# Kernel tuning notes

Measured on AMD Instinct MI355X. Metric: run time of the kernel, lower is better.

## Reference

```python
import jax, jax.numpy as jnp
import numpy as np

EPS = 1e-5
HID = 32
FUSED = 33 * 33 * 33  # 35937


def _subnet(x, gamma, beta, W1, b1, W2, b2, W3, b3):
    # BatchNorm1d in training mode: batch mean / biased variance
    mu = jnp.mean(x, axis=0)
    var = jnp.mean((x - mu) ** 2, axis=0)
    xn = (x - mu) / jnp.sqrt(var + EPS) * gamma + beta
    h = jax.nn.relu(xn @ W1 + b1)
    h = jax.nn.relu(h @ W2 + b2)
    return jax.nn.relu(h @ W3 + b3)


def _subnet_params(key, in_dim):
    ks = jax.random.split(key, 6)
    s_in = 1.0 / np.sqrt(in_dim)
    s_h = 1.0 / np.sqrt(HID)
    return dict(
        gamma=jnp.ones((in_dim,), jnp.float32),
        beta=jnp.zeros((in_dim,), jnp.float32),
        W1=jax.random.uniform(ks[0], (in_dim, HID), jnp.float32, -s_in, s_in),
        b1=jax.random.uniform(ks[1], (HID,), jnp.float32, -s_in, s_in),
        W2=jax.random.uniform(ks[2], (HID, HID), jnp.float32, -s_h, s_h),
        b2=jax.random.uniform(ks[3], (HID,), jnp.float32, -s_h, s_h),
        W3=jax.random.uniform(ks[4], (HID, HID), jnp.float32, -s_h, s_h),
        b3=jax.random.uniform(ks[5], (HID,), jnp.float32, -s_h, s_h),
    )


def setup_inputs() -> dict:
    key = jax.random.key(0)
    ks = jax.random.split(key, 10)
    B = 8192
    inp = {
        'US_x': jax.random.normal(ks[0], (B, 1024), jnp.float32),
        'CDFI_x': jax.random.normal(ks[1], (B, 1024), jnp.float32),
        'marker_x': jax.random.normal(ks[2], (B, 10), jnp.float32),
    }
    for pref, k, d in (('us', ks[3], 1024), ('cd', ks[4], 1024), ('mk', ks[5], 10)):
        for n, v in _subnet_params(k, d).items():
            inp[f'{pref}_{n}'] = v
    s1 = 1.0 / np.sqrt(FUSED)
    s2 = 1.0 / np.sqrt(33)
    inp['Wf1'] = jax.random.uniform(ks[6], (FUSED, 33), jnp.float32, -s1, s1)
    inp['bf1'] = jax.random.uniform(ks[7], (33,), jnp.float32, -s1, s1)
    inp['Wf2'] = jax.random.uniform(ks[8], (33, 5), jnp.float32, -s2, s2)
    inp['bf2'] = jax.random.uniform(ks[9], (5,), jnp.float32, -s2, s2)
    return inp


def reference(US_x, CDFI_x, marker_x,
              us_gamma, us_beta, us_W1, us_b1, us_W2, us_b2, us_W3, us_b3,
              cd_gamma, cd_beta, cd_W1, cd_b1, cd_W2, cd_b2, cd_W3, cd_b3,
              mk_gamma, mk_beta, mk_W1, mk_b1, mk_W2, mk_b2, mk_W3, mk_b3,
              Wf1, bf1, Wf2, bf2):
    B = US_x.shape[0]
    us_h = _subnet(US_x, us_gamma, us_beta, us_W1, us_b1, us_W2, us_b2, us_W3, us_b3)
    cd_h = _subnet(CDFI_x, cd_gamma, cd_beta, cd_W1, cd_b1, cd_W2, cd_b2, cd_W3, cd_b3)
    mk_h = _subnet(marker_x, mk_gamma, mk_beta, mk_W1, mk_b1, mk_W2, mk_b2, mk_W3, mk_b3)
    ones = jnp.ones((B, 1), jnp.float32)
    us1 = jnp.concatenate([ones, us_h], axis=1)   # [B,33]
    cd1 = jnp.concatenate([ones, cd_h], axis=1)   # [B,33]
    mk1 = jnp.concatenate([ones, mk_h], axis=1)   # [B,33]
    # fused[b,k,j,i] = mk1[b,k] * cd1[b,j] * us1[b,i]; flattened row-major
    fused = jnp.einsum('bk,bj,bi->bkji', mk1, cd1, us1).reshape(B, FUSED)
    h = jax.nn.relu(fused @ Wf1 + bf1)
    return jax.nn.sigmoid(h @ Wf2 + bf2)
```

## Files before the change

kernel.cpp:

```cpp
#include <hip/hip_runtime.h>
#include <hip/hip_bf16.h>
#include <math.h>

typedef __hip_bfloat16 bf16;
typedef __attribute__((ext_vector_type(4))) float f32x4;
typedef __attribute__((ext_vector_type(8))) short s16x8;

#define NB 8192
#define KP 1152
#define NP 1152
#define NK 36


struct SubP {
    const float* x; const float* gamma; const float* beta;
    const float* W1; const float* b1; const float* W2; const float* b2;
    const float* W3; const float* b3;
    float* sum; float* sumsq; float* a; float* b1p; float* hout;
    int F;
};
struct SubP3 { SubP s[3]; };

__global__ void __launch_bounds__(256) stats3_kernel(SubP3 P) {
    const SubP p = P.s[blockIdx.z];
    int t = threadIdx.x;
    int row0 = blockIdx.x * 64;
    if (p.F == 1024) {
        f32x4 s = {0.f, 0.f, 0.f, 0.f}, s2 = {0.f, 0.f, 0.f, 0.f};
        const float* xp = p.x + (size_t)row0 * 1024 + t * 4;
        #pragma unroll 8
        for (int r = 0; r < 64; r++) {
            f32x4 v = *(const f32x4*)(xp + (size_t)r * 1024);
            s += v; s2 += v * v;
        }
        int f = t * 4;
        #pragma unroll
        for (int e = 0; e < 4; e++) {
            atomicAdd(&p.sum[f + e], s[e]);
            atomicAdd(&p.sumsq[f + e], s2[e]);
        }
    } else {
        __shared__ float ls[16], ls2[16];
        if (t < 16) { ls[t] = 0.f; ls2[t] = 0.f; }
        __syncthreads();
        int F = p.F;
        for (int idx = t; idx < 64 * F; idx += 256) {
            float v = p.x[(size_t)row0 * F + idx];
            int f = idx % 10;
            atomicAdd(&ls[f], v);
            atomicAdd(&ls2[f], v * v);
        }
        __syncthreads();
        if (t < F) { atomicAdd(&p.sum[t], ls[t]); atomicAdd(&p.sumsq[t], ls2[t]); }
    }
}

__global__ void prep3_kernel(SubP3 P) {
    const SubP p = P.s[blockIdx.y];
    int f0 = blockIdx.x * 32;
    if (f0 >= p.F) return;
    int t = threadIdx.x;
    __shared__ float c_sh[32];
    __shared__ float red[8][33];
    int fc = p.F - f0; if (fc > 32) fc = 32;
    if (t < 32) {
        float c = 0.f;
        if (t < fc) {
            int f = f0 + t;
            float mu  = p.sum[f]   * (1.f / 8192.f);
            float var = p.sumsq[f] * (1.f / 8192.f) - mu * mu;
            float a = p.gamma[f] * rsqrtf(var + 1e-5f);
            p.a[f] = a;
            c = p.beta[f] - mu * a;
        }
        c_sh[t] = c;
    }
    __syncthreads();
    int h = t & 31, g = t >> 5;
    float s = 0.f;
    for (int fi = g; fi < fc; fi += 8)
        s += c_sh[fi] * p.W1[(size_t)(f0 + fi) * 32 + h];
    red[g][h] = s;
    __syncthreads();
    if (t < 32) {
        float tot = 0.f;
        #pragma unroll
        for (int gg = 0; gg < 8; gg++) tot += red[gg][t];
        atomicAdd(&p.b1p[t], tot);
    }
}

__global__ void __launch_bounds__(256) subnet3_kernel(SubP3 P) {
    const SubP p = P.s[blockIdx.y];
    const int F = p.F;
    __shared__ float smem[8832];
    float* Red = smem;
    float* H1  = smem + 3456;
    float* W23 = smem + 4608;
    float* H2  = smem;

    int t = threadIdx.x;
    int row0 = blockIdx.x * 32;
    int kg = t >> 6;
    int lane = t & 63;
    int hg = lane & 7, h0 = hg * 4;
    int rg = (lane >> 3) & 3;
    int ks = lane >> 5;

    float acc[4][8] = {};

    if (F == 1024) {
        float* Xt = smem;
        float* Wt = smem + 4224;
        int xr = t >> 3, xc = (t & 7) * 16;
        int wk = t >> 1, wh = (t & 1) * 16;
        const float* xbase = p.x + (size_t)row0 * 1024;
        f32x4 xp[4], wp[4]; float av;
        #pragma unroll
        for (int i = 0; i < 4; i++) xp[i] = *(const f32x4*)&xbase[(size_t)xr * 1024 + xc + i * 4];
        #pragma unroll
        for (int i = 0; i < 4; i++) wp[i] = *(const f32x4*)&p.W1[(size_t)wk * 32 + wh + i * 4];
        av = p.a[wk];
        int kb = (kg * 2 + ks) * 16;
        for (int c = 0; c < 8; c++) {
            __syncthreads();
            #pragma unroll
            for (int i = 0; i < 4; i++) *(f32x4*)&Xt[xr * 132 + xc + i * 4] = xp[i];
            #pragma unroll
            for (int i = 0; i < 4; i++) *(f32x4*)&Wt[wk * 36 + wh + i * 4] = wp[i] * av;
            if (c < 7) {
                int k0 = (c + 1) * 128;
                #pragma unroll
                for (int i = 0; i < 4; i++) xp[i] = *(const f32x4*)&xbase[(size_t)xr * 1024 + k0 + xc + i * 4];
                #pragma unroll
                for (int i = 0; i < 4; i++) wp[i] = *(const f32x4*)&p.W1[(size_t)(k0 + wk) * 32 + wh + i * 4];
                av = p.a[k0 + wk];
            }
            __syncthreads();
            #pragma unroll
            for (int s = 0; s < 4; s++) {
                int kk = kb + s * 4;
                f32x4 wv[4], xv[8];
                #pragma unroll
                for (int j = 0; j < 4; j++)  wv[j]  = *(const f32x4*)&Wt[(kk + j) * 36 + h0];
                #pragma unroll
                for (int ri = 0; ri < 8; ri++) xv[ri] = *(const f32x4*)&Xt[(rg + 4 * ri) * 132 + kk];
                #pragma unroll
                for (int j = 0; j < 4; j++)
                    #pragma unroll
                    for (int hi = 0; hi < 4; hi++) {
                        float w = wv[j][hi];
                        #pragma unroll
                        for (int ri = 0; ri < 8; ri++)
                            acc[hi][ri] = fmaf(w, xv[ri][j], acc[hi][ri]);
                    }
            }
        }
    } else {
        float* Xt = smem;
        float* Wt = smem + 2176;
        int kbase = (kg * 2 + ks) * 8;
        for (int k0 = 0; k0 < F; k0 += 64) {
            int kc = F - k0; if (kc > 64) kc = 64;
            int kcp = (kc + 3) & ~3;
            __syncthreads();
            for (int idx = t; idx < 32 * kcp; idx += 256) {
                int r = idx / kcp, kk = idx - r * kcp;
                Xt[r * 68 + kk] = (kk < kc) ? p.x[(size_t)(row0 + r) * F + k0 + kk] : 0.f;
            }
            for (int idx = t; idx < kcp * 32; idx += 256) {
                int kk = idx >> 5, hh = idx & 31;
                Wt[kk * 36 + hh] = (kk < kc) ? p.a[k0 + kk] * p.W1[(size_t)(k0 + kk) * 32 + hh] : 0.f;
            }
            __syncthreads();
            #pragma unroll
            for (int s = 0; s < 2; s++) {
                int kk = kbase + s * 4;
                if (kk < kcp) {
                    f32x4 wv[4], xv[8];
                    #pragma unroll
                    for (int j = 0; j < 4; j++)  wv[j]  = *(const f32x4*)&Wt[(kk + j) * 36 + h0];
                    #pragma unroll
                    for (int ri = 0; ri < 8; ri++) xv[ri] = *(const f32x4*)&Xt[(rg + 4 * ri) * 68 + kk];
                    #pragma unroll
                    for (int j = 0; j < 4; j++)
                        #pragma unroll
                        for (int hi = 0; hi < 4; hi++) {
                            float w = wv[j][hi];
                            #pragma unroll
                            for (int ri = 0; ri < 8; ri++)
                                acc[hi][ri] = fmaf(w, xv[ri][j], acc[hi][ri]);
                        }
                }
            }
        }
    }
    #pragma unroll
    for (int hi = 0; hi < 4; hi++)
        #pragma unroll
        for (int ri = 0; ri < 8; ri++)
            acc[hi][ri] += __shfl_xor(acc[hi][ri], 32);
    __syncthreads();
    if (kg > 0 && ks == 0) {
        #pragma unroll
        for (int ri = 0; ri < 8; ri++) {
            int r = rg + 4 * ri;
            f32x4 v = {acc[0][ri], acc[1][ri], acc[2][ri], acc[3][ri]};
            *(f32x4*)&Red[(kg - 1) * 1152 + r * 36 + h0] = v;
        }
    }
    for (int idx = t; idx < 1024; idx += 256) W23[(idx >> 5) * 33 + (idx & 31)] = p.W2[idx];
    __syncthreads();
    if (kg == 0 && ks == 0) {
        f32x4 b;
        #pragma unroll
        for (int hi = 0; hi < 4; hi++) b[hi] = p.b1[h0 + hi] + p.b1p[h0 + hi];
        #pragma unroll
        for (int ri = 0; ri < 8; ri++) {
            int r = rg + 4 * ri;
            f32x4 v = {acc[0][ri], acc[1][ri], acc[2][ri], acc[3][ri]};
            #pragma unroll
            for (int pp = 0; pp < 3; pp++)
                v += *(const f32x4*)&Red[pp * 1152 + r * 36 + h0];
            v += b;
            #pragma unroll
            for (int hi = 0; hi < 4; hi++)
                H1[r * 36 + h0 + hi] = fmaxf(v[hi], 0.f);
        }
    }
    __syncthreads();
    int h = t & 31, rq = t >> 5;
    {
        float a2[4] = {};
        for (int q = 0; q < 32; q++) {
            float w = W23[q * 33 + h];
            #pragma unroll
            for (int i = 0; i < 4; i++) a2[i] += H1[(rq * 4 + i) * 36 + q] * w;
        }
        float bv = p.b2[h];
        #pragma unroll
        for (int i = 0; i < 4; i++) H2[(rq * 4 + i) * 36 + h] = fmaxf(a2[i] + bv, 0.f);
    }
    __syncthreads();
    for (int idx = t; idx < 1024; idx += 256) W23[(idx >> 5) * 33 + (idx & 31)] = p.W3[idx];
    __syncthreads();
    {
        float a3[4] = {};
        for (int q = 0; q < 32; q++) {
            float w = W23[q * 33 + h];
            #pragma unroll
            for (int i = 0; i < 4; i++) a3[i] += H2[(rq * 4 + i) * 36 + q] * w;
        }
        float bv = p.b3[h];
        #pragma unroll
        for (int i = 0; i < 4; i++)
            p.hout[(size_t)(row0 + rq * 4 + i) * 32 + h] = fmaxf(a3[i] + bv, 0.f);
    }
}

__global__ void build_both(const float* __restrict__ mk_h, const float* __restrict__ us_h,
                           bf16* __restrict__ p1,
                           const float* __restrict__ Wf1, bf16* __restrict__ W2t) {
    int blk = blockIdx.x;
    int t = threadIdx.x;
    if (blk < NB) {
        int b = blk;
        __shared__ float mk1[33], us1[33];
        if (t == 0) { mk1[0] = 1.f; us1[0] = 1.f; }
        if (t < 32) mk1[t + 1] = mk_h[(size_t)b * 32 + t];
        else if (t < 64) us1[t - 31] = us_h[(size_t)b * 32 + (t - 32)];
        __syncthreads();
        if (t < 144) {
            int base = t * 8;
            s16x8 v;
            #pragma unroll
            for (int e = 0; e < 8; e++) {
                int idx = base + e;
                float val = 0.f;
                if (idx < 1089) {
                    int k = idx / 33, i = idx - k * 33;
                    val = mk1[k] * us1[i];
                }
                __hip_bfloat16 hb = __float2bfloat16(val);
                v[e] = *(short*)&hb;
            }
            int mb = b >> 7, rr = b & 127;
            int h = rr >> 6, mt = (rr >> 4) & 3, fr = rr & 15;
            size_t fo = ((size_t)(mb * 36 + (t >> 2)) * 8 + h * 4 + mt) * 64 + (t & 3) * 16 + fr;
            *(s16x8*)(p1 + fo * 8) = v;
        }
    } else {
        int kj = blk - NB;
        int k = kj / 33, j = kj - k * 33;
        __shared__ float tile[1089];
        const float* src = Wf1 + (size_t)k * 35937 + (size_t)j * 1089;
        for (int idx = t; idx < 1089; idx += 192) tile[idx] = src[idx];
        __syncthreads();
        for (int idx = t; idx < 1089; idx += 192) {
            int o = idx / 33, i = idx - o * 33;
            int R = j * 33 + o;
            int C = k * 33 + i;
            int nb = R >> 7, rr = R & 127;
            int hb = rr >> 6, nt = (rr >> 4) & 3, fr = rr & 15;
            int kss = C >> 5, q = (C >> 3) & 3, e = C & 7;
            size_t fo = ((size_t)(nb * 36 + kss) * 8 + hb * 4 + nt) * 64 + q * 16 + fr;
            W2t[fo * 8 + e] = __float2bfloat16(tile[i * 33 + o]);
        }
        if (k == 0) {
            bf16 z = __float2bfloat16(0.f);
            for (int idx = t; idx < 33 * 63; idx += 192) {
                int o = idx / 63, C = 1089 + idx - o * 63;
                int R = j * 33 + o;
                int nb = R >> 7, rr = R & 127;
                int hb = rr >> 6, nt = (rr >> 4) & 3, fr = rr & 15;
                int kss = C >> 5, q = (C >> 3) & 3, e = C & 7;
                size_t fo = ((size_t)(nb * 36 + kss) * 8 + hb * 4 + nt) * 64 + q * 16 + fr;
                W2t[fo * 8 + e] = z;
            }
        }
    }
}

__global__ void __launch_bounds__(256) gemm_kernel(const bf16* __restrict__ pA,
                                                   const bf16* __restrict__ pB,
                                                   bf16* __restrict__ S) {
    int t = threadIdx.x;
    int mb = blockIdx.x, nb = blockIdx.y;
    int wave = t >> 6, lane = t & 63;
    int h = wave & 1, hb = wave >> 1;
    int wm = h * 64, wn = hb * 64;

    const s16x8* Ap = (const s16x8*)pA + ((size_t)mb * 36 * 8 + h * 4) * 64 + lane;
    const s16x8* Bp = (const s16x8*)pB + ((size_t)nb * 36 * 8 + hb * 4) * 64 + lane;

    f32x4 acc[4][4] = {};
    s16x8 a0[4], b0[4], a1[4], b1[4];

    #pragma unroll
    for (int mt = 0; mt < 4; mt++) a0[mt] = Ap[mt * 64];
    #pragma unroll
    for (int nt = 0; nt < 4; nt++) b0[nt] = Bp[nt * 64];

    for (int ks = 0; ks < NK; ks += 2) {
        #pragma unroll
        for (int mt = 0; mt < 4; mt++) a1[mt] = Ap[(ks + 1) * 512 + mt * 64];
        #pragma unroll
        for (int nt = 0; nt < 4; nt++) b1[nt] = Bp[(ks + 1) * 512 + nt * 64];
        #pragma unroll
        for (int mt = 0; mt < 4; mt++)
            #pragma unroll
            for (int nt = 0; nt < 4; nt++)
                acc[mt][nt] = __builtin_amdgcn_mfma_f32_16x16x32_bf16(a0[mt], b0[nt], acc[mt][nt], 0, 0, 0);
        if (ks + 2 < NK) {
            #pragma unroll
            for (int mt = 0; mt < 4; mt++) a0[mt] = Ap[(ks + 2) * 512 + mt * 64];
            #pragma unroll
            for (int nt = 0; nt < 4; nt++) b0[nt] = Bp[(ks + 2) * 512 + nt * 64];
        }
        #pragma unroll
        for (int mt = 0; mt < 4; mt++)
            #pragma unroll
            for (int nt = 0; nt < 4; nt++)
                acc[mt][nt] = __builtin_amdgcn_mfma_f32_16x16x32_bf16(a1[mt], b1[nt], acc[mt][nt], 0, 0, 0);
    }

    int col = lane & 15, rowg = (lane >> 4) * 4;
    int m0 = mb * 128, n0 = nb * 128;
    #pragma unroll
    for (int mt = 0; mt < 4; mt++)
        #pragma unroll
        for (int nt = 0; nt < 4; nt++)
            #pragma unroll
            for (int r = 0; r < 4; r++) {
                int gr = m0 + wm + mt * 16 + rowg + r;
                int gc = n0 + wn + nt * 16 + col;
                S[(size_t)gr * NP + gc] = __float2bfloat16(acc[mt][nt][r]);
            }
}

__global__ void __launch_bounds__(256) epilogue_kernel(const bf16* __restrict__ S,
                                const float* __restrict__ cd_h,
                                const float* __restrict__ bf1, const float* __restrict__ Wf2,
                                const float* __restrict__ bf2, float* __restrict__ out) {
    int w = threadIdx.x >> 6;
    int lane = threadIdx.x & 63;
    int b = blockIdx.x * 4 + w;
    __shared__ __align__(16) unsigned short Sl[4][1152];
    __shared__ float cdsh[4][33];
    __shared__ float hsh[4][40];
    const bf16* Srow = S + (size_t)b * NP;
    #pragma unroll
    for (int pass = 0; pass < 3; pass++) {
        int idx = lane + pass * 64;
        if (idx < 144)
            *(s16x8*)&Sl[w][idx * 8] = *(const s16x8*)(Srow + idx * 8);
    }
    if (lane == 0) cdsh[w][0] = 1.f;
    if (lane < 32) cdsh[w][lane + 1] = cd_h[(size_t)b * 32 + lane];
    __syncthreads();
    if (lane < 33) {
        float acc = bf1[lane];
        #pragma unroll 3
        for (int j = 0; j < 33; j++) {
            unsigned short sv = Sl[w][j * 33 + lane];
            acc += cdsh[w][j] * __bfloat162float(*(bf16*)&sv);
        }
        hsh[w][lane] = fmaxf(acc, 0.f);
    }
    __syncthreads();
    if (lane < 5) {
        float o = bf2[lane];
        for (int q = 0; q < 33; q++) o += hsh[w][q] * Wf2[q * 5 + lane];
        out[(size_t)b * 5 + lane] = 1.f / (1.f + expf(-o));
    }
}

extern "C" void kernel_launch(void* const* d_in, const int* in_sizes, int n_in,
                              void* d_out, int out_size, void* d_ws, size_t ws_size,
                              hipStream_t stream) {
    const float* US_x     = (const float*)d_in[0];
    const float* CDFI_x   = (const float*)d_in[1];
    const float* marker_x = (const float*)d_in[2];
    const float* Wf1      = (const float*)d_in[27];
    const float* bf1      = (const float*)d_in[28];
    const float* Wf2      = (const float*)d_in[29];
    const float* bf2      = (const float*)d_in[30];
    float* out = (float*)d_out;

    char* ws = (char*)d_ws;
    size_t off = 0;
    auto alloc = [&](size_t bytes) -> void* {
        void* p = ws + off;
        off = (off + bytes + 255) & ~(size_t)255;
        return p;
    };

    float* stat_big = (float*)alloc(3 * 2176 * sizeof(float));
    float* a_buf[3], *h_buf[3];
    for (int i = 0; i < 3; i++) {
        a_buf[i] = (float*)alloc(1024 * 4);
        h_buf[i] = (float*)alloc((size_t)NB * 32 * 4);
    }
    bf16*  p1   = (bf16*)alloc((size_t)NB * KP * 2);
    bf16*  W2t  = (bf16*)alloc((size_t)NP * KP * 2);
    bf16*  S    = (bf16*)alloc((size_t)NB * NP * 2);

    SubP3 P;
    const float* xs[3] = {US_x, CDFI_x, marker_x};
    int Fs[3] = {1024, 1024, 10};
    for (int i = 0; i < 3; i++) {
        int base = 3 + i * 8;
        P.s[i].x     = xs[i];
        P.s[i].gamma = (const float*)d_in[base + 0];
        P.s[i].beta  = (const float*)d_in[base + 1];
        P.s[i].W1    = (const float*)d_in[base + 2];
        P.s[i].b1    = (const float*)d_in[base + 3];
        P.s[i].W2    = (const float*)d_in[base + 4];
        P.s[i].b2    = (const float*)d_in[base + 5];
        P.s[i].W3    = (const float*)d_in[base + 6];
        P.s[i].b3    = (const float*)d_in[base + 7];
        P.s[i].sum   = stat_big + i * 2176;
        P.s[i].sumsq = stat_big + i * 2176 + 1024;
        P.s[i].b1p   = stat_big + i * 2176 + 2048;
        P.s[i].a     = a_buf[i];
        P.s[i].hout  = h_buf[i];
        P.s[i].F     = Fs[i];
    }

    float* us_h = h_buf[0];
    float* cd_h = h_buf[1];
    float* mk_h = h_buf[2];

    hipMemsetAsync(stat_big, 0, 3 * 2176 * sizeof(float), stream);

    stats3_kernel<<<dim3(128, 1, 3), 256, 0, stream>>>(P);
    prep3_kernel<<<dim3(32, 3), 256, 0, stream>>>(P);
    subnet3_kernel<<<dim3(256, 3), 256, 0, stream>>>(P);

    build_both<<<NB + 1089, 192, 0, stream>>>(mk_h, us_h, p1, Wf1, W2t);

    gemm_kernel<<<dim3(NB / 128, NP / 128), 256, 0, stream>>>(p1, W2t, S);

    epilogue_kernel<<<NB / 4, 256, 0, stream>>>(S, cd_h, bf1, Wf2, bf2, out);
}
```

Before: 276.9 us.

## Fuse GEMM with epilogue and replace stat atomics with per-block partials

The GEMM now gives each block 32 rows and the full 1152-wide N dimension, stages the bf16 result tile in shared memory and runs the cd contraction, ReLU, second linear layer and sigmoid in the same kernel. This removes the intermediate S buffer round-trip to global memory and one kernel launch. The A and B packed layouts are changed to suit the new tiling. BatchNorm statistics are written as per-block partial sums and reduced in prep3, replacing global float atomics. In exchange the new tiling re-reads the whole B matrix per block, lowers occupancy through large accumulators and shared memory, and runs only 256 blocks.

```diff
diff --git a/kernel.cpp b/kernel.cpp
--- a/kernel.cpp
+++ b/kernel.cpp
@@ -24,7 +24,8 @@
 __global__ void __launch_bounds__(256) stats3_kernel(SubP3 P) {
     const SubP p = P.s[blockIdx.z];
     int t = threadIdx.x;
-    int row0 = blockIdx.x * 64;
+    int blk = blockIdx.x;
+    int row0 = blk * 64;
     if (p.F == 1024) {
         f32x4 s = {0.f, 0.f, 0.f, 0.f}, s2 = {0.f, 0.f, 0.f, 0.f};
         const float* xp = p.x + (size_t)row0 * 1024 + t * 4;
@@ -34,11 +35,8 @@
             s += v; s2 += v * v;
         }
         int f = t * 4;
-        #pragma unroll
-        for (int e = 0; e < 4; e++) {
-            atomicAdd(&p.sum[f + e], s[e]);
-            atomicAdd(&p.sumsq[f + e], s2[e]);
-        }
+        *(f32x4*)&p.sum[(size_t)blk * 2048 + f]   = s;
+        *(f32x4*)&p.sumsq[(size_t)blk * 2048 + f] = s2;
     } else {
         __shared__ float ls[16], ls2[16];
         if (t < 16) { ls[t] = 0.f; ls2[t] = 0.f; }
@@ -51,7 +49,10 @@
             atomicAdd(&ls2[f], v * v);
         }
         __syncthreads();
-        if (t < F) { atomicAdd(&p.sum[t], ls[t]); atomicAdd(&p.sumsq[t], ls2[t]); }
+        if (t < F) {
+            p.sum[(size_t)blk * 2048 + t]   = ls[t];
+            p.sumsq[(size_t)blk * 2048 + t] = ls2[t];
+        }
     }
 }
 
@@ -62,13 +63,29 @@
     int t = threadIdx.x;
     __shared__ float c_sh[32];
     __shared__ float red[8][33];
+    __shared__ float rs[8][33], rs2[8][33];
     int fc = p.F - f0; if (fc > 32) fc = 32;
+    int fi = t & 31, g = t >> 5;
+    {
+        float s = 0.f, s2 = 0.f;
+        if (fi < fc) {
+            for (int blk = g; blk < 128; blk += 8) {
+                s  += p.sum[(size_t)blk * 2048 + f0 + fi];
+                s2 += p.sumsq[(size_t)blk * 2048 + f0 + fi];
+            }
+        }
+        rs[g][fi] = s; rs2[g][fi] = s2;
+    }
+    __syncthreads();
     if (t < 32) {
         float c = 0.f;
         if (t < fc) {
+            float sm = 0.f, sq = 0.f;
+            #pragma unroll
+            for (int gg = 0; gg < 8; gg++) { sm += rs[gg][t]; sq += rs2[gg][t]; }
             int f = f0 + t;
-            float mu  = p.sum[f]   * (1.f / 8192.f);
-            float var = p.sumsq[f] * (1.f / 8192.f) - mu * mu;
+            float mu  = sm * (1.f / 8192.f);
+            float var = sq * (1.f / 8192.f) - mu * mu;
             float a = p.gamma[f] * rsqrtf(var + 1e-5f);
             p.a[f] = a;
             c = p.beta[f] - mu * a;
@@ -76,10 +93,10 @@
         c_sh[t] = c;
     }
     __syncthreads();
-    int h = t & 31, g = t >> 5;
+    int h = t & 31; g = t >> 5;
     float s = 0.f;
-    for (int fi = g; fi < fc; fi += 8)
-        s += c_sh[fi] * p.W1[(size_t)(f0 + fi) * 32 + h];
+    for (int fi2 = g; fi2 < fc; fi2 += 8)
+        s += c_sh[fi2] * p.W1[(size_t)(f0 + fi2) * 32 + h];
     red[g][h] = s;
     __syncthreads();
     if (t < 32) {
@@ -284,9 +301,8 @@
                 __hip_bfloat16 hb = __float2bfloat16(val);
                 v[e] = *(short*)&hb;
             }
-            int mb = b >> 7, rr = b & 127;
-            int h = rr >> 6, mt = (rr >> 4) & 3, fr = rr & 15;
-            size_t fo = ((size_t)(mb * 36 + (t >> 2)) * 8 + h * 4 + mt) * 64 + (t & 3) * 16 + fr;
+            int m16 = b >> 4, fr = b & 15;
+            size_t fo = ((size_t)(t >> 2) * 512 + m16) * 64 + (t & 3) * 16 + fr;
             *(s16x8*)(p1 + fo * 8) = v;
         }
     } else {
@@ -300,10 +316,9 @@
             int o = idx / 33, i = idx - o * 33;
             int R = j * 33 + o;
             int C = k * 33 + i;
-            int nb = R >> 7, rr = R & 127;
-            int hb = rr >> 6, nt = (rr >> 4) & 3, fr = rr & 15;
+            int fn = R >> 4, fr = R & 15;
             int kss = C >> 5, q = (C >> 3) & 3, e = C & 7;
-            size_t fo = ((size_t)(nb * 36 + kss) * 8 + hb * 4 + nt) * 64 + q * 16 + fr;
+            size_t fo = ((size_t)kss * 72 + fn) * 64 + q * 16 + fr;
             W2t[fo * 8 + e] = __float2bfloat16(tile[i * 33 + o]);
         }
         if (k == 0) {
@@ -311,107 +326,95 @@
             for (int idx = t; idx < 33 * 63; idx += 192) {
                 int o = idx / 63, C = 1089 + idx - o * 63;
                 int R = j * 33 + o;
-                int nb = R >> 7, rr = R & 127;
-                int hb = rr >> 6, nt = (rr >> 4) & 3, fr = rr & 15;
+                int fn = R >> 4, fr = R & 15;
                 int kss = C >> 5, q = (C >> 3) & 3, e = C & 7;
-                size_t fo = ((size_t)(nb * 36 + kss) * 8 + hb * 4 + nt) * 64 + q * 16 + fr;
+                size_t fo = ((size_t)kss * 72 + fn) * 64 + q * 16 + fr;
                 W2t[fo * 8 + e] = z;
             }
         }
     }
 }
 
-__global__ void __launch_bounds__(256) gemm_kernel(const bf16* __restrict__ pA,
-                                                   const bf16* __restrict__ pB,
-                                                   bf16* __restrict__ S) {
+__global__ void __launch_bounds__(256, 2) gemm_fused(const bf16* __restrict__ pA,
+                                                     const bf16* __restrict__ pB,
+                                                     const float* __restrict__ cd_h,
+                                                     const float* __restrict__ bf1,
+                                                     const float* __restrict__ Wf2,
+                                                     const float* __restrict__ bf2,
+                                                     float* __restrict__ out) {
+    __shared__ __align__(16) unsigned short Sl[32 * 1156];
+    __shared__ float cdl[32][33];
     int t = threadIdx.x;
-    int mb = blockIdx.x, nb = blockIdx.y;
+    int bid = blockIdx.x;
+    int m0 = bid * 32;
     int wave = t >> 6, lane = t & 63;
-    int h = wave & 1, hb = wave >> 1;
-    int wm = h * 64, wn = hb * 64;
-
-    const s16x8* Ap = (const s16x8*)pA + ((size_t)mb * 36 * 8 + h * 4) * 64 + lane;
-    const s16x8* Bp = (const s16x8*)pB + ((size_t)nb * 36 * 8 + hb * 4) * 64 + lane;
-
-    f32x4 acc[4][4] = {};
-    s16x8 a0[4], b0[4], a1[4], b1[4];
-
+    int wn = wave;
+
+    for (int u = t; u < 32 * 33; u += 256) {
+        int row = u / 33, j = u - row * 33;
+        cdl[row][j] = (j == 0) ? 1.f : cd_h[(size_t)(m0 + row) * 32 + (j - 1)];
+    }
+
+    const s16x8* Ap = (const s16x8*)pA;
+    const s16x8* Bp = (const s16x8*)pB;
+
+    f32x4 acc[2][18] = {};
+
+    for (int ks = 0; ks < NK; ks++) {
+        size_t ab = ((size_t)ks * 512 + bid * 2) * 64 + lane;
+        s16x8 af0 = Ap[ab];
+        s16x8 af1 = Ap[ab + 64];
+        #pragma unroll
+        for (int hh = 0; hh < 2; hh++) {
+            size_t bb = ((size_t)ks * 72 + wn * 18 + hh * 9) * 64 + lane;
+            s16x8 bf[9];
+            #pragma unroll
+            for (int nt = 0; nt < 9; nt++) bf[nt] = Bp[bb + nt * 64];
+            #pragma unroll
+            for (int nt = 0; nt < 9; nt++) {
+                int n2 = hh * 9 + nt;
+                acc[0][n2] = __builtin_amdgcn_mfma_f32_16x16x32_bf16(af0, bf[nt], acc[0][n2], 0, 0, 0);
+                acc[1][n2] = __builtin_amdgcn_mfma_f32_16x16x32_bf16(af1, bf[nt], acc[1][n2], 0, 0, 0);
+            }
+        }
+    }
+
+    int col = lane & 15, rowg = (lane >> 4) * 4;
     #pragma unroll
-    for (int mt = 0; mt < 4; mt++) a0[mt] = Ap[mt * 64];
-    #pragma unroll
-    for (int nt = 0; nt < 4; nt++) b0[nt] = Bp[nt * 64];
-
-    for (int ks = 0; ks < NK; ks += 2) {
-        #pragma unroll
-        for (int mt = 0; mt < 4; mt++) a1[mt] = Ap[(ks + 1) * 512 + mt * 64];
-        #pragma unroll
-        for (int nt = 0; nt < 4; nt++) b1[nt] = Bp[(ks + 1) * 512 + nt * 64];
-        #pragma unroll
-        for (int mt = 0; mt < 4; mt++)
-            #pragma unroll
-            for (int nt = 0; nt < 4; nt++)
-                acc[mt][nt] = __builtin_amdgcn_mfma_f32_16x16x32_bf16(a0[mt], b0[nt], acc[mt][nt], 0, 0, 0);
-        if (ks + 2 < NK) {
-            #pragma unroll
-            for (int mt = 0; mt < 4; mt++) a0[mt] = Ap[(ks + 2) * 512 + mt * 64];
-            #pragma unroll
-            for (int nt = 0; nt < 4; nt++) b0[nt] = Bp[(ks + 2) * 512 + nt * 64];
-        }
-        #pragma unroll
-        for (int mt = 0; mt < 4; mt++)
-            #pragma unroll
-            for (int nt = 0; nt < 4; nt++)
-                acc[mt][nt] = __builtin_amdgcn_mfma_f32_16x16x32_bf16(a1[mt], b1[nt], acc[mt][nt], 0, 0, 0);
-    }
-
-    int col = lane & 15, rowg = (lane >> 4) * 4;
-    int m0 = mb * 128, n0 = nb * 128;
-    #pragma unroll
-    for (int mt = 0; mt < 4; mt++)
-        #pragma unroll
-        for (int nt = 0; nt < 4; nt++)
+    for (int mt = 0; mt < 2; mt++)
+        #pragma unroll
+        for (int n2 = 0; n2 < 18; n2++)
             #pragma unroll
             for (int r = 0; r < 4; r++) {
-                int gr = m0 + wm + mt * 16 + rowg + r;
-                int gc = n0 + wn + nt * 16 + col;
-                S[(size_t)gr * NP + gc] = __float2bfloat16(acc[mt][nt][r]);
-            }
-}
-
-__global__ void __launch_bounds__(256) epilogue_kernel(const bf16* __restrict__ S,
-                                const float* __restrict__ cd_h,
-                                const float* __restrict__ bf1, const float* __restrict__ Wf2,
-                                const float* __restrict__ bf2, float* __restrict__ out) {
-    int w = threadIdx.x >> 6;
-    int lane = threadIdx.x & 63;
-    int b = blockIdx.x * 4 + w;
-    __shared__ __align__(16) unsigned short Sl[4][1152];
-    __shared__ float cdsh[4][33];
-    __shared__ float hsh[4][40];
-    const bf16* Srow = S + (size_t)b * NP;
-    #pragma unroll
-    for (int pass = 0; pass < 3; pass++) {
-        int idx = lane + pass * 64;
-        if (idx < 144)
-            *(s16x8*)&Sl[w][idx * 8] = *(const s16x8*)(Srow + idx * 8);
-    }
-    if (lane == 0) cdsh[w][0] = 1.f;
-    if (lane < 32) cdsh[w][lane + 1] = cd_h[(size_t)b * 32 + lane];
-    __syncthreads();
-    if (lane < 33) {
-        float acc = bf1[lane];
+                int lrow = mt * 16 + rowg + r;
+                int lcol = wn * 288 + n2 * 16 + col;
+                __hip_bfloat16 hb = __float2bfloat16(acc[mt][n2][r]);
+                Sl[lrow * 1156 + lcol] = *(unsigned short*)&hb;
+            }
+    __syncthreads();
+
+    float hreg[5];
+    int nh = 0;
+    for (int u = t; u < 32 * 33; u += 256, nh++) {
+        int row = u / 33, o = u - row * 33;
+        float a = bf1[o];
         #pragma unroll 3
         for (int j = 0; j < 33; j++) {
-            unsigned short sv = Sl[w][j * 33 + lane];
-            acc += cdsh[w][j] * __bfloat162float(*(bf16*)&sv);
-        }
-        hsh[w][lane] = fmaxf(acc, 0.f);
-    }
-    __syncthreads();
-    if (lane < 5) {
-        float o = bf2[lane];
-        for (int q = 0; q < 33; q++) o += hsh[w][q] * Wf2[q * 5 + lane];
-        out[(size_t)b * 5 + lane] = 1.f / (1.f + expf(-o));
+            unsigned short sv = Sl[row * 1156 + j * 33 + o];
+            a += cdl[row][j] * __bfloat162float(*(bf16*)&sv);
+        }
+        hreg[nh] = fmaxf(a, 0.f);
+    }
+    __syncthreads();
+    float* hsh = (float*)&Sl[0];
+    nh = 0;
+    for (int u = t; u < 32 * 33; u += 256, nh++) hsh[u] = hreg[nh];
+    __syncthreads();
+    if (t < 160) {
+        int row = t / 5, o2 = t - row * 5;
+        float v = bf2[o2];
+        for (int q = 0; q < 33; q++) v += hsh[row * 33 + q] * Wf2[q * 5 + o2];
+        out[(size_t)(m0 + row) * 5 + o2] = 1.f / (1.f + expf(-v));
     }
 }
 
@@ -435,7 +438,8 @@
         return p;
     };
 
-    float* stat_big = (float*)alloc(3 * 2176 * sizeof(float));
+    float* b1p_buf  = (float*)alloc(3 * 128 * sizeof(float));
+    float* pstat    = (float*)alloc(3 * 128 * 2048 * sizeof(float));
     float* a_buf[3], *h_buf[3];
     for (int i = 0; i < 3; i++) {
         a_buf[i] = (float*)alloc(1024 * 4);
@@ -443,7 +447,6 @@
     }
     bf16*  p1   = (bf16*)alloc((size_t)NB * KP * 2);
     bf16*  W2t  = (bf16*)alloc((size_t)NP * KP * 2);
-    bf16*  S    = (bf16*)alloc((size_t)NB * NP * 2);
 
     SubP3 P;
     const float* xs[3] = {US_x, CDFI_x, marker_x};
@@ -459,9 +462,9 @@
         P.s[i].b2    = (const float*)d_in[base + 5];
         P.s[i].W3    = (const float*)d_in[base + 6];
         P.s[i].b3    = (const float*)d_in[base + 7];
-        P.s[i].sum   = stat_big + i * 2176;
-        P.s[i].sumsq = stat_big + i * 2176 + 1024;
-        P.s[i].b1p   = stat_big + i * 2176 + 2048;
+        P.s[i].sum   = pstat + (size_t)i * 128 * 2048;
+        P.s[i].sumsq = pstat + (size_t)i * 128 * 2048 + 1024;
+        P.s[i].b1p   = b1p_buf + i * 128;
         P.s[i].a     = a_buf[i];
         P.s[i].hout  = h_buf[i];
         P.s[i].F     = Fs[i];
@@ -471,7 +474,7 @@
     float* cd_h = h_buf[1];
     float* mk_h = h_buf[2];
 
-    hipMemsetAsync(stat_big, 0, 3 * 2176 * sizeof(float), stream);
+    hipMemsetAsync(b1p_buf, 0, 3 * 128 * sizeof(float), stream);
 
     stats3_kernel<<<dim3(128, 1, 3), 256, 0, stream>>>(P);
     prep3_kernel<<<dim3(32, 3), 256, 0, stream>>>(P);
@@ -479,7 +482,5 @@
 
     build_both<<<NB + 1089, 192, 0, stream>>>(mk_h, us_h, p1, Wf1, W2t);
 
-    gemm_kernel<<<dim3(NB / 128, NP / 128), 256, 0, stream>>>(p1, W2t, S);
-
-    epilogue_kernel<<<NB / 4, 256, 0, stream>>>(S, cd_h, bf1, Wf2, bf2, out);
-}
+    gemm_fused<<<NB / 32, 256, 0, stream>>>(p1, W2t, cd_h, bf1, Wf2, bf2, out);
+}
```

Result: slower. 321.8 us (+16.2%).
